# Kernel optimization log

Measured on AMD Instinct MI355X. Metric: run time of the kernel, lower is better.

The kernel has to match this reference:

```python
import jax, jax.numpy as jnp
import numpy as np

VOCAB = 1_000_000
EMBED_DIM = 64
INIT_STD = 0.01


def setup_inputs() -> dict:
    key = jax.random.key(0)
    k_tab, k_idx = jax.random.split(key)
    # dense materialization of the dict-based KV store: N(mean=0, std=0.01)
    table = jax.random.normal(k_tab, (VOCAB, EMBED_DIM), dtype=jnp.float32) * INIT_STD
    indices = jax.random.randint(k_idx, (4096, 200), 0, VOCAB, dtype=jnp.int64)
    dummy = jnp.zeros((1,), dtype=jnp.float32)  # _grad_dummy parameter
    return {"indices": indices, "table": table, "dummy": dummy}


def reference(indices, table, dummy):
    # Faithful to KVEmbeddingFunction.forward: unique->fetch->inverse-gather is
    # mathematically a plain row gather; + dummy.sum()*0.0 keeps the grad path.
    out = table[indices]  # [B, L, D]
    return out + dummy.sum() * 0.0
```

## Files before the change

### kernel.cpp

```cpp
#include <hip/hip_runtime.h>


typedef float f32x4 __attribute__((ext_vector_type(4)));

__global__ __launch_bounds__(256) void kv_gather_kernel(
    const int* __restrict__ idx,
    const float* __restrict__ table,
    float* __restrict__ out)
{
    const long long i = (long long)blockIdx.x * blockDim.x + threadIdx.x;
    const long long row = i >> 4;
    const int sub = (int)(i & 15);
    const long long t = (long long)idx[row];
    const f32x4* __restrict__ src = reinterpret_cast<const f32x4*>(table + t * 64);
    f32x4* __restrict__ dst = reinterpret_cast<f32x4*>(out + row * 64);
    dst[sub] = src[sub];
}

extern "C" void kernel_launch(void* const* d_in, const int* in_sizes, int n_in,
                              void* d_out, int out_size, void* d_ws, size_t ws_size,
                              hipStream_t stream)
{
    const int*   idx   = (const int*)d_in[0];
    const float* table = (const float*)d_in[1];
    float*       out   = (float*)d_out;

    const long long nrows = in_sizes[0];
    const long long total = nrows << 4;
    const int block = 256;
    const long long nblk = (total + block - 1) / block;

    kv_gather_kernel<<<(int)nblk, block, 0, stream>>>(idx, table, out);
}
```

Baseline: 76.71 us.

## Batch index loads ahead of row gathers in a persistent grid-stride kernel

Replaces the one-element-per-thread gather with a fixed 2048-block grid where each thread first loads 25 indices, then issues 25 dependent 16-byte row copies. The goal is more memory-level parallelism, since index latency is taken once per batch rather than once per element, and lower block launch overhead. A fast path is used only when the total exactly matches the hardcoded shape (819200 rows); other sizes fall back to a grid-stride kernel. The unrolled arrays raise register use and may lower occupancy.

```diff
diff --git a/kernel.cpp b/kernel.cpp
--- a/kernel.cpp
+++ b/kernel.cpp
@@ -3,18 +3,55 @@
 
 typedef float f32x4 __attribute__((ext_vector_type(4)));
 
-__global__ __launch_bounds__(256) void kv_gather_kernel(
+constexpr int  BLOCK  = 256;
+constexpr int  NBLK   = 2048;
+constexpr int  ITERS  = 25;
+constexpr long long STRIDE = (long long)NBLK * BLOCK;
+
+__global__ __launch_bounds__(BLOCK) void kv_gather_pipelined(
     const int* __restrict__ idx,
     const float* __restrict__ table,
     float* __restrict__ out)
 {
-    const long long i = (long long)blockIdx.x * blockDim.x + threadIdx.x;
-    const long long row = i >> 4;
-    const int sub = (int)(i & 15);
-    const long long t = (long long)idx[row];
-    const f32x4* __restrict__ src = reinterpret_cast<const f32x4*>(table + t * 64);
-    f32x4* __restrict__ dst = reinterpret_cast<f32x4*>(out + row * 64);
-    dst[sub] = src[sub];
+    const long long i0 = (long long)blockIdx.x * BLOCK + threadIdx.x;
+
+    int t[ITERS];
+#pragma unroll
+    for (int k = 0; k < ITERS; ++k) {
+        const long long i = i0 + (long long)k * STRIDE;
+        t[k] = idx[i >> 4];
+    }
+
+#pragma unroll
+    for (int k = 0; k < ITERS; ++k) {
+        const long long i   = i0 + (long long)k * STRIDE;
+        const long long row = i >> 4;
+        const int       sub = (int)(i & 15);
+        const f32x4* __restrict__ src =
+            reinterpret_cast<const f32x4*>(table + (long long)t[k] * 64);
+        f32x4* __restrict__ dst = reinterpret_cast<f32x4*>(out + row * 64);
+        dst[sub] = src[sub];
+    }
+}
+
+__global__ __launch_bounds__(BLOCK) void kv_gather_generic(
+    const int* __restrict__ idx,
+    const float* __restrict__ table,
+    float* __restrict__ out,
+    long long nrows)
+{
+    const long long total = nrows << 4;
+    long long i = (long long)blockIdx.x * blockDim.x + threadIdx.x;
+    const long long stride = (long long)gridDim.x * blockDim.x;
+    for (; i < total; i += stride) {
+        const long long row = i >> 4;
+        const int sub = (int)(i & 15);
+        const long long t = (long long)idx[row];
+        const f32x4* __restrict__ src =
+            reinterpret_cast<const f32x4*>(table + t * 64);
+        f32x4* __restrict__ dst = reinterpret_cast<f32x4*>(out + row * 64);
+        dst[sub] = src[sub];
+    }
 }
 
 extern "C" void kernel_launch(void* const* d_in, const int* in_sizes, int n_in,
@@ -27,8 +64,12 @@
 
     const long long nrows = in_sizes[0];
     const long long total = nrows << 4;
-    const int block = 256;
-    const long long nblk = (total + block - 1) / block;
 
-    kv_gather_kernel<<<(int)nblk, block, 0, stream>>>(idx, table, out);
+    if (total == STRIDE * ITERS) {
+        kv_gather_pipelined<<<NBLK, BLOCK, 0, stream>>>(idx, table, out);
+    } else {
+        long long nblk = (total + BLOCK - 1) / BLOCK;
+        if (nblk > NBLK) nblk = NBLK;
+        kv_gather_generic<<<(int)nblk, BLOCK, 0, stream>>>(idx, table, out, nrows);
+    }
 }
```

Result: faster. 74.61 us (-2.7%).
